# Kernel tuning notes

Hardware: AMD Instinct MI355X
Metric: run time of the kernel (lower is better)

Reference implementation:

```python
import jax, jax.numpy as jnp
import numpy as np

N = 100000
E = 1600000
H = 128
IN = 16
OUT = 16
L = 3
G = 256  # number of graphs
EPS = 1e-12


def setup_inputs() -> dict:
    key = jax.random.key(0)
    ks = jax.random.split(key, 24)
    s = 0.05
    inp = {
        "x": jax.random.normal(ks[0], (N, IN), jnp.float32),
        "pos": jax.random.normal(ks[1], (N, 3), jnp.float32),
        "edge_index": jax.random.randint(ks[2], (2, E), 0, N, jnp.int64),
        "batch": jnp.sort(jax.random.randint(ks[3], (N,), 0, G, jnp.int64)),
        # node_lin: Linear(IN,H), ReLU, Linear(H,H)
        "node_W1": jax.random.normal(ks[4], (IN, H), jnp.float32) * s,
        "node_b1": jnp.zeros((H,), jnp.float32),
        "node_W2": jax.random.normal(ks[5], (H, H), jnp.float32) * s,
        "node_b2": jnp.zeros((H,), jnp.float32),
        # per-layer local_nn: Linear(H+4,H), ReLU, Linear(H,H)  (stacked over L)
        "local_W1": jax.random.normal(ks[6], (L, H + 4, H), jnp.float32) * s,
        "local_b1": jnp.zeros((L, H), jnp.float32),
        "local_W2": jax.random.normal(ks[7], (L, H, H), jnp.float32) * s,
        "local_b2": jnp.zeros((L, H), jnp.float32),
        # per-layer global_nn: Linear(H,H), ReLU, Linear(H,H)
        "global_W1": jax.random.normal(ks[8], (L, H, H), jnp.float32) * s,
        "global_b1": jnp.zeros((L, H), jnp.float32),
        "global_W2": jax.random.normal(ks[9], (L, H, H), jnp.float32) * s,
        "global_b2": jnp.zeros((L, H), jnp.float32),
        # heads
        "lin1_W": jax.random.normal(ks[10], (H, H // 2), jnp.float32) * s,
        "lin1_b": jnp.zeros((H // 2,), jnp.float32),
        "lin2_W": jax.random.normal(ks[11], (H // 2, OUT), jnp.float32) * s,
        "lin2_b": jnp.zeros((OUT,), jnp.float32),
    }
    return inp


def _angle(v1, v2):
    c = jnp.cross(v1, v2, axis=1)
    return jnp.arctan2(jnp.linalg.norm(c, axis=1), jnp.sum(v1 * v2, axis=1))


def reference(x, pos, edge_index, batch,
              node_W1, node_b1, node_W2, node_b2,
              local_W1, local_b1, local_W2, local_b2,
              global_W1, global_b1, global_W2, global_b2,
              lin1_W, lin1_b, lin2_W, lin2_b):
    src = edge_index[0]  # j (source)
    dst = edge_index[1]  # i (target, aggregation index)

    normal = pos / (jnp.linalg.norm(pos, axis=-1, keepdims=True) + EPS)

    pos_i, pos_j = pos[dst], pos[src]
    n_i, n_j = normal[dst], normal[src]
    pseudo = pos_j - pos_i  # [E, 3]
    # point-pair features [E, 4] (constant across layers since pos is fixed)
    ppf = jnp.stack([
        jnp.linalg.norm(pseudo, axis=1),
        _angle(n_i, pseudo),
        _angle(n_j, pseudo),
        _angle(n_i, n_j),
    ], axis=1)

    # node_lin (x is 2D -> MLP path; embedding path unused)
    h = jax.nn.relu(x @ node_W1 + node_b1) @ node_W2 + node_b2  # [N, H]

    for l in range(L):
        msg = jnp.concatenate([h[src], ppf], axis=1)  # [E, H+4]
        msg = jax.nn.relu(msg @ local_W1[l] + local_b1[l]) @ local_W2[l] + local_b2[l]
        agg = jax.ops.segment_sum(msg, dst, num_segments=N)  # scatter-add to nodes
        h = jax.nn.relu(agg @ global_W1[l] + global_b1[l]) @ global_W2[l] + global_b2[l]
        h = jax.nn.relu(h)

    out = jax.nn.relu(h @ lin1_W + lin1_b) @ lin2_W + lin2_b  # [N, OUT]
    return jax.ops.segment_sum(out, batch, num_segments=G)  # [G, OUT]
```

## Files before the change

kernel.cpp:

```cpp
#include <hip/hip_runtime.h>

#define NN 100000
#define NE 1600000
#define HD 128
#define NL 3
#define NG 256
#define NB 196
#define BCAP 56

typedef __attribute__((ext_vector_type(8))) short short8;
typedef __attribute__((ext_vector_type(4))) float floatx4;
typedef __attribute__((ext_vector_type(2))) _Float16 half2v;

static __device__ __forceinline__ unsigned short f2bf(float f) {
    unsigned int u = __float_as_uint(f);
    u += 0x7fffu + ((u >> 16) & 1u);
    return (unsigned short)(u >> 16);
}
static __device__ __forceinline__ float bf2f(unsigned short h) {
    return __uint_as_float(((unsigned int)h) << 16);
}
static __device__ __forceinline__ float angle3(float ax, float ay, float az,
                                               float bx, float by, float bz) {
    float cx = ay*bz - az*by;
    float cy = az*bx - ax*bz;
    float cz = ax*by - ay*bx;
    float cn = sqrtf(cx*cx + cy*cy + cz*cz);
    float d  = ax*bx + ay*by + az*bz;
    return atan2f(cn, d);
}

union U32H2 { unsigned int u; half2v h; };
static __device__ __forceinline__ half2v u2h(unsigned int x) { U32H2 t; t.u = x; return t.h; }
static __device__ __forceinline__ unsigned int h2u(half2v x) { U32H2 t; t.h = x; return t.u; }


struct PrepSrcs { const float* p[14]; };

__global__ void k_prep(PrepSrcs s, unsigned short* __restrict__ dst) {
    int mat = blockIdx.y;
    int N = (mat == 13) ? 64 : 128;
    int e = blockIdx.x * 256 + threadIdx.x;
    if (e >= N * 128) return;
    int n = e >> 7, k = e & 127;
    dst[mat * 16384 + n * 128 + k] = f2bf(s.p[mat][k * N + n]);
}


__global__ void k_pn(const float* __restrict__ pos, float4* __restrict__ pn, int n) {
    int i = blockIdx.x * blockDim.x + threadIdx.x;
    if (i >= n) return;
    float x = pos[3*i], y = pos[3*i+1], z = pos[3*i+2];
    float inv = 1.0f / (sqrtf(x*x + y*y + z*z) + 1e-12f);
    pn[2*i]   = make_float4(x, y, z, 0.0f);
    pn[2*i+1] = make_float4(x*inv, y*inv, z*inv, 0.0f);
}


__global__ __launch_bounds__(256) void k_bcount(const int* __restrict__ ei,
                                                int* __restrict__ bcnt, int e) {
    __shared__ int cnt[NB];
    int tid = threadIdx.x;
    for (int i = tid; i < NB; i += 256) cnt[i] = 0;
    __syncthreads();
    int i0 = blockIdx.x * 4096 + tid * 16;
    if (i0 < e) {
#pragma unroll
        for (int q = 0; q < 4; q++) {
            int4 d4 = *(const int4*)(ei + NE + i0 + q * 4);
            atomicAdd(&cnt[d4.x >> 9], 1);
            atomicAdd(&cnt[d4.y >> 9], 1);
            atomicAdd(&cnt[d4.z >> 9], 1);
            atomicAdd(&cnt[d4.w >> 9], 1);
        }
    }
    __syncthreads();
    for (int i = tid; i < NB; i += 256)
        if (cnt[i]) atomicAdd(&bcnt[i], cnt[i]);
}

__global__ void k_bscan(const int* __restrict__ bcnt, int* __restrict__ bbase,
                        int* __restrict__ bcursor, int* __restrict__ starts) {
    if (threadIdx.x == 0 && blockIdx.x == 0) {
        int acc = 0;
        for (int b = 0; b < NB; b++) {
            bbase[b] = acc; bcursor[b] = acc;
            acc += bcnt[b];
        }
        bbase[NB] = acc;
        starts[NN] = NE;
    }
}

__global__ __launch_bounds__(256) void k_bscatter(const int* __restrict__ ei,
                                                  int* __restrict__ bcursor,
                                                  unsigned int* __restrict__ bids, int e) {
    __shared__ int lcnt[NB];
    __shared__ unsigned int lbuf[NB * BCAP];
    int tid = threadIdx.x;
    for (int i = tid; i < NB; i += 256) lcnt[i] = 0;
    __syncthreads();
    int i0 = blockIdx.x * 4096 + tid * 16;
    if (i0 < e) {
#pragma unroll
        for (int q = 0; q < 4; q++) {
            int4 s4 = *(const int4*)(ei + i0 + q * 4);
            int4 d4 = *(const int4*)(ei + NE + i0 + q * 4);
            int ds[4] = {d4.x, d4.y, d4.z, d4.w};
            int ss[4] = {s4.x, s4.y, s4.z, s4.w};
#pragma unroll
            for (int r = 0; r < 4; r++) {
                int d = ds[r];
                int b = d >> 9;
                unsigned int w = ((unsigned int)(d & 511) << 17) | (unsigned int)ss[r];
                int pos = atomicAdd(&lcnt[b], 1);
                if (pos < BCAP) lbuf[b * BCAP + pos] = w;
                else { int p = atomicAdd(&bcursor[b], 1); bids[p] = w; }
            }
        }
    }
    __syncthreads();
    if (tid < NB) {
        int c = lcnt[tid];
        if (c > BCAP) c = BCAP;
        if (c > 0) {
            int base = atomicAdd(&bcursor[tid], c);
            for (int k = 0; k < c; k++) bids[base + k] = lbuf[tid * BCAP + k];
        }
    }
}

__global__ __launch_bounds__(256) void k_bfinal(const unsigned int* __restrict__ bids,
                                                const int* __restrict__ bbase,
                                                int* __restrict__ ssrc,
                                                int* __restrict__ sdst,
                                                int* __restrict__ starts,
                                                int* __restrict__ deg) {
    __shared__ int s1[512];
    __shared__ int s2[256];
    int tid = threadIdx.x;
    int b = blockIdx.x;
    int node0 = b << 9;
    int base0 = bbase[b];
    int cnt = bbase[b + 1] - base0;
    s1[2 * tid] = 0; s1[2 * tid + 1] = 0;
    __syncthreads();
    for (int j = tid; j < cnt; j += 256)
        atomicAdd(&s1[bids[base0 + j] >> 17], 1);
    __syncthreads();
    int a0 = s1[2 * tid], a1 = s1[2 * tid + 1];
    s2[tid] = a0 + a1;
    __syncthreads();
    for (int off = 1; off < 256; off <<= 1) {
        int v = (tid >= off) ? s2[tid - off] : 0;
        __syncthreads();
        s2[tid] += v;
        __syncthreads();
    }
    int pairBase = (tid ? s2[tid - 1] : 0);
    int e0 = base0 + pairBase;
    int e1 = e0 + a0;
    int n0 = node0 + 2 * tid;
    if (n0 < NN)     { starts[n0] = e0;     deg[n0] = a0; }
    if (n0 + 1 < NN) { starts[n0 + 1] = e1; deg[n0 + 1] = a1; }
    s1[2 * tid] = e0; s1[2 * tid + 1] = e1;
    __syncthreads();
    for (int j = tid; j < cnt; j += 256) {
        unsigned int w = bids[base0 + j];
        int loc = w >> 17;
        int src = (int)(w & 0x1ffffu);
        int p = atomicAdd(&s1[loc], 1);
        ssrc[p] = src;
        sdst[p] = node0 + loc;
    }
}

__global__ void k_ppf_sorted(const int* __restrict__ ssrc, const int* __restrict__ sdst,
                             const float4* __restrict__ pn,
                             uint2* __restrict__ sppf, int e) {
    int j = blockIdx.x * blockDim.x + threadIdx.x;
    if (j >= e) return;
    int s = ssrc[j];
    int d = sdst[j];
    float4 ps_ = pn[2*s], ns_ = pn[2*s+1];
    float4 pd_ = pn[2*d], nd_ = pn[2*d+1];
    float px = ps_.x - pd_.x;
    float py = ps_.y - pd_.y;
    float pz = ps_.z - pd_.z;
    float f0 = sqrtf(px*px + py*py + pz*pz);
    float f1 = angle3(nd_.x, nd_.y, nd_.z, px, py, pz);
    float f2 = angle3(ns_.x, ns_.y, ns_.z, px, py, pz);
    float f3 = angle3(nd_.x, nd_.y, nd_.z, ns_.x, ns_.y, ns_.z);
    half2v h01 = { (_Float16)f0, (_Float16)f1 };
    half2v h23 = { (_Float16)f2, (_Float16)f3 };
    uint2 w;
    w.x = h2u(h01);
    w.y = h2u(h23);
    sppf[j] = w;
}


__global__ void k_node_lin1(const float* __restrict__ x, const float* __restrict__ W1,
                            const float* __restrict__ b1, unsigned short* __restrict__ u, int n) {
    __shared__ float sW[16 * HD];
    __shared__ float sb[HD];
    __shared__ float sx[16 * 16];
    int tid = threadIdx.x;
    for (int idx = tid; idx < 16 * HD; idx += 256) sW[idx] = W1[idx];
    if (tid < HD) sb[tid] = b1[tid];
    int r0 = blockIdx.x * 16;
    for (int idx = tid; idx < 16 * 16; idx += 256) {
        int r = r0 + (idx >> 4);
        sx[idx] = (r < n) ? x[r * 16 + (idx & 15)] : 0.0f;
    }
    __syncthreads();
    int col = tid & 127;
    int rsub = tid >> 7;
    float wcol[16];
#pragma unroll
    for (int k = 0; k < 16; k++) wcol[k] = sW[k * HD + col];
    float bb = sb[col];
    for (int rr = rsub; rr < 16; rr += 2) {
        int r = r0 + rr;
        if (r >= n) break;
        float acc = bb;
#pragma unroll
        for (int k = 0; k < 16; k++) acc = fmaf(sx[rr * 16 + k], wcol[k], acc);
        u[r * HD + col] = f2bf(fmaxf(acc, 0.0f));
    }
}


template <int NC, int EPI>
__global__ __launch_bounds__(256, 2) void k_gemm128(
    const unsigned short* __restrict__ A, const unsigned short* __restrict__ Wt,
    const float* __restrict__ bias, const int* __restrict__ deg,
    const float* __restrict__ b2, unsigned short* __restrict__ out, int n) {
    constexpr int SK = 136;
    __shared__ unsigned short Bt[NC * SK];
    int tid = threadIdx.x;
    for (int idx = tid; idx < NC * 16; idx += 256) {
        int c = idx >> 4, k8 = idx & 15;
        *(short8*)&Bt[c * SK + k8 * 8] = ((const short8*)Wt)[idx];
    }
    __syncthreads();

    int wave = tid >> 6, lane = tid & 63;
    int quad = lane >> 4, m = lane & 15;
    int rowBase = blockIdx.x * 128 + wave * 32;

    short8 a[2][4];
#pragma unroll
    for (int rt = 0; rt < 2; rt++) {
        int r = rowBase + rt * 16 + m;
        int rc = (r < n) ? r : (n - 1);
        const unsigned short* ap = A + (size_t)rc * 128 + quad * 8;
#pragma unroll
        for (int s = 0; s < 4; s++) a[rt][s] = *(const short8*)(ap + s * 32);
    }

    constexpr int NT = NC / 16;
    floatx4 acc[2][NT];
    floatx4 z = {0.0f, 0.0f, 0.0f, 0.0f};
#pragma unroll
    for (int rt = 0; rt < 2; rt++)
#pragma unroll
        for (int ct = 0; ct < NT; ct++) acc[rt][ct] = z;

#pragma unroll
    for (int ct = 0; ct < NT; ct++) {
        const unsigned short* bp = &Bt[(ct * 16 + m) * SK + quad * 8];
#pragma unroll
        for (int s = 0; s < 4; s++) {
            short8 b = *(const short8*)(bp + s * 32);
            acc[0][ct] = __builtin_amdgcn_mfma_f32_16x16x32_bf16(a[0][s], b, acc[0][ct], 0, 0, 0);
            acc[1][ct] = __builtin_amdgcn_mfma_f32_16x16x32_bf16(a[1][s], b, acc[1][ct], 0, 0, 0);
        }
    }

    float dv[2][4];
    if (EPI == 2) {
#pragma unroll
        for (int rt = 0; rt < 2; rt++)
#pragma unroll
            for (int r = 0; r < 4; r++) {
                int orow = rowBase + rt * 16 + quad * 4 + r;
                dv[rt][r] = (orow < n) ? (float)deg[orow] : 0.0f;
            }
    }

#pragma unroll
    for (int ct = 0; ct < NT; ct++) {
        int col = ct * 16 + m;
        float bv = (EPI == 0) ? 0.0f : ((EPI == 2) ? b2[col] : bias[col]);
#pragma unroll
        for (int rt = 0; rt < 2; rt++) {
#pragma unroll
            for (int r = 0; r < 4; r++) {
                int orow = rowBase + rt * 16 + quad * 4 + r;
                if (orow < n) {
                    float v = acc[rt][ct][r];
                    if (EPI == 1 || EPI == 3) v += bv;
                    if (EPI == 2) v += dv[rt][r] * bv;
                    if (EPI == 3) v = fmaxf(v, 0.0f);
                    out[(size_t)orow * NC + col] = f2bf(v);
                }
            }
        }
    }
}


#define SKW 136
#define SKT 136

__global__ __launch_bounds__(256, 2) void k_gchain(
    const unsigned short* __restrict__ S, const unsigned short* __restrict__ W2t,
    const unsigned short* __restrict__ GW1t, const unsigned short* __restrict__ GW2t,
    const int* __restrict__ deg, const float* __restrict__ b2,
    const float* __restrict__ Gb1, const float* __restrict__ Gb2,
    unsigned short* __restrict__ out, int n) {
    __shared__ unsigned short LW[128 * SKW];
    __shared__ unsigned short LT[128 * SKT];
    __shared__ float sb2[128], sg1[128], sg2[128];
    int tid = threadIdx.x;
    if (tid < 128) { sb2[tid] = b2[tid]; sg1[tid] = Gb1[tid]; sg2[tid] = Gb2[tid]; }
    int wave = tid >> 6, lane = tid & 63, quad = lane >> 4, m = lane & 15;
    int rowBase = wave * 32;
    int gBase = blockIdx.x * 128;
    int rowC = rowBase + quad * 4;
    const unsigned short* Ws[3] = {W2t, GW1t, GW2t};
    floatx4 z = {0.0f, 0.0f, 0.0f, 0.0f};
    short8 a[2][4];
#pragma unroll
    for (int rt = 0; rt < 2; rt++) {
        int r = gBase + rowBase + rt * 16 + m;
        int rc = r < n ? r : n - 1;
        const unsigned short* ap = S + (size_t)rc * 128 + quad * 8;
#pragma unroll
        for (int s = 0; s < 4; s++) a[rt][s] = *(const short8*)(ap + s * 32);
    }
    float dvd[2][4];
#pragma unroll
    for (int rt = 0; rt < 2; rt++)
#pragma unroll
        for (int r = 0; r < 4; r++) {
            int gr = gBase + rowBase + rt * 16 + quad * 4 + r;
            dvd[rt][r] = (float)deg[gr < n ? gr : n - 1];
        }

#pragma unroll
    for (int st = 0; st < 3; st++) {
        for (int idx = tid; idx < 128 * 16; idx += 256) {
            int c = idx >> 4, k8 = idx & 15;
            *(short8*)&LW[c * SKW + k8 * 8] = ((const short8*)Ws[st])[idx];
        }
        if (st > 0) {
#pragma unroll
            for (int rt = 0; rt < 2; rt++) {
                const unsigned short* tp = &LT[(rowBase + rt * 16 + m) * SKT + quad * 8];
#pragma unroll
                for (int s = 0; s < 4; s++) a[rt][s] = *(const short8*)(tp + s * 32);
            }
        }
        __syncthreads();

        floatx4 acc[2][8];
#pragma unroll
        for (int rt = 0; rt < 2; rt++)
#pragma unroll
            for (int ct = 0; ct < 8; ct++) acc[rt][ct] = z;
#pragma unroll
        for (int ct = 0; ct < 8; ct++) {
            const unsigned short* bp = &LW[(ct * 16 + m) * SKW + quad * 8];
#pragma unroll
            for (int s = 0; s < 4; s++) {
                short8 b = *(const short8*)(bp + s * 32);
                acc[0][ct] = __builtin_amdgcn_mfma_f32_16x16x32_bf16(a[0][s], b, acc[0][ct], 0, 0, 0);
                acc[1][ct] = __builtin_amdgcn_mfma_f32_16x16x32_bf16(a[1][s], b, acc[1][ct], 0, 0, 0);
            }
        }
#pragma unroll
        for (int ct = 0; ct < 8; ct++) {
            int col = ct * 16 + m;
            float bb = (st == 0) ? sb2[col] : (st == 1 ? sg1[col] : sg2[col]);
#pragma unroll
            for (int rt = 0; rt < 2; rt++) {
#pragma unroll
                for (int r = 0; r < 4; r++) {
                    float v = acc[rt][ct][r];
                    if (st == 0) v += dvd[rt][r] * bb;
                    else v = fmaxf(v + bb, 0.0f);
                    int row = rowBase + rt * 16 + quad * 4 + r;
                    if (st < 2) {
                        LT[row * SKT + col] = f2bf(v);
                    } else {
                        int gr = gBase + row;
                        if (gr < n) out[(size_t)gr * 128 + col] = f2bf(v);
                    }
                }
            }
        }
        __syncthreads();
    }
}


#if __has_builtin(__builtin_amdgcn_fdot2)
#define HAVE_FDOT2 1
#else
#define HAVE_FDOT2 0
#endif

static __device__ __forceinline__ void agg_edge(unsigned int u, uint2 q,
                                                half2v wA0, half2v wB0, half2v wA1, half2v wB1,
                                                float2 bb, float& a0, float& a1) {
    float tlo = __uint_as_float(u << 16);
    float thi = __uint_as_float(u & 0xffff0000u);
#if HAVE_FDOT2
    half2v p01 = u2h(q.x), p23 = u2h(q.y);
    float g0 = __builtin_amdgcn_fdot2(p01, wA0,
               __builtin_amdgcn_fdot2(p23, wB0, bb.x + tlo, false), false);
    float g1 = __builtin_amdgcn_fdot2(p01, wA1,
               __builtin_amdgcn_fdot2(p23, wB1, bb.y + thi, false), false);
#else
    half2v p01 = u2h(q.x), p23 = u2h(q.y);
    float px = (float)p01.x, py = (float)p01.y, pz = (float)p23.x, pw = (float)p23.y;
    float g0 = fmaf(px, (float)wA0.x, fmaf(py, (float)wA0.y,
               fmaf(pz, (float)wB0.x, fmaf(pw, (float)wB0.y, bb.x + tlo))));
    float g1 = fmaf(px, (float)wA1.x, fmaf(py, (float)wA1.y,
               fmaf(pz, (float)wB1.x, fmaf(pw, (float)wB1.y, bb.y + thi))));
#endif
    a0 += fmaxf(g0, 0.0f);
    a1 += fmaxf(g1, 0.0f);
}

__global__ __launch_bounds__(256, 8) void k_agg(
    const int* __restrict__ starts, const int* __restrict__ ssrc,
    const uint2* __restrict__ sppf, const unsigned int* __restrict__ t,
    const float* __restrict__ W1p, const float* __restrict__ b1,
    unsigned int* __restrict__ S, int n) {
    int node = (blockIdx.x * 256 + threadIdx.x) >> 6;
    if (node >= n) return;
    int lane = threadIdx.x & 63;
    int c2 = lane * 2;
    float2 w0 = *(const float2*)(W1p + c2);
    float2 w1 = *(const float2*)(W1p + 128 + c2);
    float2 w2 = *(const float2*)(W1p + 256 + c2);
    float2 w3 = *(const float2*)(W1p + 384 + c2);
    float2 bb = *(const float2*)(b1 + c2);
    half2v wA0 = { (_Float16)w0.x, (_Float16)w1.x };
    half2v wB0 = { (_Float16)w2.x, (_Float16)w3.x };
    half2v wA1 = { (_Float16)w0.y, (_Float16)w1.y };
    half2v wB1 = { (_Float16)w2.y, (_Float16)w3.y };
    int e0 = __builtin_amdgcn_readfirstlane(starts[node]);
    int e1 = __builtin_amdgcn_readfirstlane(starts[node + 1]);
    float a0 = 0.0f, a1 = 0.0f;
    int e = e0;
    for (; e + 8 <= e1; e += 8) {
        int s0 = ssrc[e],     s1 = ssrc[e + 1], s2 = ssrc[e + 2], s3 = ssrc[e + 3];
        int s4 = ssrc[e + 4], s5 = ssrc[e + 5], s6 = ssrc[e + 6], s7 = ssrc[e + 7];
        uint2 q0 = sppf[e],     q1 = sppf[e + 1], q2 = sppf[e + 2], q3 = sppf[e + 3];
        uint2 q4 = sppf[e + 4], q5 = sppf[e + 5], q6 = sppf[e + 6], q7 = sppf[e + 7];
        unsigned int u0 = t[((unsigned)s0 << 6) | lane];
        unsigned int u1 = t[((unsigned)s1 << 6) | lane];
        unsigned int u2 = t[((unsigned)s2 << 6) | lane];
        unsigned int u3 = t[((unsigned)s3 << 6) | lane];
        unsigned int u4 = t[((unsigned)s4 << 6) | lane];
        unsigned int u5 = t[((unsigned)s5 << 6) | lane];
        unsigned int u6 = t[((unsigned)s6 << 6) | lane];
        unsigned int u7 = t[((unsigned)s7 << 6) | lane];
        agg_edge(u0, q0, wA0, wB0, wA1, wB1, bb, a0, a1);
        agg_edge(u1, q1, wA0, wB0, wA1, wB1, bb, a0, a1);
        agg_edge(u2, q2, wA0, wB0, wA1, wB1, bb, a0, a1);
        agg_edge(u3, q3, wA0, wB0, wA1, wB1, bb, a0, a1);
        agg_edge(u4, q4, wA0, wB0, wA1, wB1, bb, a0, a1);
        agg_edge(u5, q5, wA0, wB0, wA1, wB1, bb, a0, a1);
        agg_edge(u6, q6, wA0, wB0, wA1, wB1, bb, a0, a1);
        agg_edge(u7, q7, wA0, wB0, wA1, wB1, bb, a0, a1);
    }
    for (; e + 4 <= e1; e += 4) {
        int s0 = ssrc[e], s1 = ssrc[e + 1], s2 = ssrc[e + 2], s3 = ssrc[e + 3];
        uint2 q0 = sppf[e], q1 = sppf[e + 1], q2 = sppf[e + 2], q3 = sppf[e + 3];
        unsigned int u0 = t[((unsigned)s0 << 6) | lane];
        unsigned int u1 = t[((unsigned)s1 << 6) | lane];
        unsigned int u2 = t[((unsigned)s2 << 6) | lane];
        unsigned int u3 = t[((unsigned)s3 << 6) | lane];
        agg_edge(u0, q0, wA0, wB0, wA1, wB1, bb, a0, a1);
        agg_edge(u1, q1, wA0, wB0, wA1, wB1, bb, a0, a1);
        agg_edge(u2, q2, wA0, wB0, wA1, wB1, bb, a0, a1);
        agg_edge(u3, q3, wA0, wB0, wA1, wB1, bb, a0, a1);
    }
    for (; e < e1; e++) {
        int s0 = ssrc[e];
        uint2 q0 = sppf[e];
        unsigned int u0 = t[((unsigned)s0 << 6) | lane];
        agg_edge(u0, q0, wA0, wB0, wA1, wB1, bb, a0, a1);
    }
    unsigned int r = ((unsigned int)f2bf(a1) << 16) | f2bf(a0);
    S[(size_t)node * 64 + lane] = r;
}


__global__ void k_head2(const unsigned short* __restrict__ v, const float* __restrict__ W,
                        const float* __restrict__ b, const int* __restrict__ batch,
                        float* __restrict__ outg, int n) {
    __shared__ float sW[64 * 16];
    __shared__ float sb[16];
    __shared__ float sacc[64][17];
    __shared__ int sbid[64];
    int tid = threadIdx.x;
    for (int idx = tid; idx < 64 * 16; idx += 256) sW[idx] = W[idx];
    if (tid < 16) sb[tid] = b[tid];
    int r0 = blockIdx.x * 64;
    if (tid < 64) {
        int r = r0 + tid;
        sbid[tid] = (r < n) ? batch[r] : -1;
    }
    __syncthreads();
    int rl = tid >> 4, c = tid & 15;
#pragma unroll
    for (int i = 0; i < 4; i++) {
        int row = rl + i * 16;
        int r = r0 + row;
        float acc = 0.0f;
        if (r < n) {
            const unsigned int* vr = (const unsigned int*)(v + (size_t)r * 64);
            acc = sb[c];
#pragma unroll
            for (int k2 = 0; k2 < 32; k2++) {
                unsigned int u = vr[k2];
                acc = fmaf(__uint_as_float(u << 16), sW[(2 * k2) * 16 + c], acc);
                acc = fmaf(__uint_as_float(u & 0xffff0000u), sW[(2 * k2 + 1) * 16 + c], acc);
            }
        }
        sacc[row][c] = acc;
    }
    __syncthreads();
    if (tid < 16) {
        int cc = tid;
        float run = 0.0f;
        int cur = sbid[0];
        for (int row = 0; row < 64; row++) {
            int bid = sbid[row];
            if (bid != cur) {
                if (cur >= 0) atomicAdd(&outg[cur * 16 + cc], run);
                run = 0.0f;
                cur = bid;
            }
            run += sacc[row][cc];
        }
        if (cur >= 0) atomicAdd(&outg[cur * 16 + cc], run);
    }
}


extern "C" void kernel_launch(void* const* d_in, const int* in_sizes, int n_in,
                              void* d_out, int out_size, void* d_ws, size_t ws_size,
                              hipStream_t stream) {
    (void)in_sizes; (void)n_in; (void)out_size; (void)ws_size;
    const float* x    = (const float*)d_in[0];
    const float* pos  = (const float*)d_in[1];
    const int*   ei   = (const int*)d_in[2];
    const int*   batch= (const int*)d_in[3];
    const float* nW1  = (const float*)d_in[4];
    const float* nb1  = (const float*)d_in[5];
    const float* nW2  = (const float*)d_in[6];
    const float* nb2  = (const float*)d_in[7];
    const float* lW1  = (const float*)d_in[8];
    const float* lb1  = (const float*)d_in[9];
    const float* lW2  = (const float*)d_in[10];
    const float* lb2  = (const float*)d_in[11];
    const float* gW1  = (const float*)d_in[12];
    const float* gb1  = (const float*)d_in[13];
    const float* gW2  = (const float*)d_in[14];
    const float* gb2  = (const float*)d_in[15];
    const float* l1W  = (const float*)d_in[16];
    const float* l1b  = (const float*)d_in[17];
    const float* l2W  = (const float*)d_in[18];
    const float* l2b  = (const float*)d_in[19];
    float* outg = (float*)d_out;

    char* ws = (char*)d_ws;
    size_t off = 0;
    auto alloc = [&](size_t bytes) -> void* {
        void* p = ws + off;
        off = (off + bytes + 255) & ~(size_t)255;
        return p;
    };
    unsigned short* P0 = (unsigned short*)alloc((size_t)NN * HD * 2);
    unsigned short* P1 = (unsigned short*)alloc((size_t)NN * HD * 2);
    uint2* sppf  = (uint2*)alloc((size_t)NE * 8);
    int* ssrc    = (int*)alloc((size_t)NE * 4);
    int* sdst    = (int*)alloc((size_t)NE * 4);
    float4* pn   = (float4*)alloc((size_t)NN * 32);
    int* deg     = (int*)alloc((size_t)NN * 4);
    int* starts  = (int*)alloc((size_t)(NN + 2) * 4);
    int* bcnt    = (int*)alloc((size_t)(NB + 2) * 4);
    int* bbase   = (int*)alloc((size_t)(NB + 2) * 4);
    int* bcursor = (int*)alloc((size_t)(NB + 2) * 4);
    unsigned short* pw = (unsigned short*)alloc((size_t)14 * 16384 * 2);
    unsigned int* bids = (unsigned int*)P0;

    PrepSrcs ps;
    ps.p[0] = nW2;
    for (int l = 0; l < 3; l++) {
        ps.p[1 + l] = lW1 + (size_t)l * 132 * 128;
        ps.p[4 + l] = lW2 + (size_t)l * 16384;
        ps.p[7 + l] = gW1 + (size_t)l * 16384;
        ps.p[10 + l] = gW2 + (size_t)l * 16384;
    }
    ps.p[13] = l1W;

    hipMemsetAsync(bcnt, 0, (size_t)(NB + 2) * 4, stream);
    hipMemsetAsync(outg, 0, (size_t)NG * 16 * 4, stream);

    k_prep<<<dim3(64, 14), 256, 0, stream>>>(ps, pw);
    k_pn<<<(NN + 255) / 256, 256, 0, stream>>>(pos, pn, NN);
    const int NTILE = (NE + 4095) / 4096;
    k_bcount<<<NTILE, 256, 0, stream>>>(ei, bcnt, NE);
    k_bscan<<<1, 64, 0, stream>>>(bcnt, bbase, bcursor, starts);
    k_bscatter<<<NTILE, 256, 0, stream>>>(ei, bcursor, bids, NE);
    k_bfinal<<<NB, 256, 0, stream>>>(bids, bbase, ssrc, sdst, starts, deg);
    k_ppf_sorted<<<(NE + 255) / 256, 256, 0, stream>>>(ssrc, sdst, pn, sppf, NE);

    k_node_lin1<<<(NN + 15) / 16, 256, 0, stream>>>(x, nW1, nb1, P1, NN);
    const int GB = (NN + 127) / 128;
    k_gemm128<128, 1><<<GB, 256, 0, stream>>>(P1, pw, nb2, nullptr, nullptr, P0, NN);

    unsigned short* hbuf = P0;
    unsigned short* obuf = P1;
    const int AGB = (NN * 64 + 255) / 256;
    for (int l = 0; l < NL; l++) {
        const float* W1p = lW1 + (size_t)l * 132 * 128 + 128 * 128;
        const float* b1  = lb1 + l * 128;
        const float* b2  = lb2 + l * 128;
        const float* Gb1 = gb1 + l * 128;
        const float* Gb2 = gb2 + l * 128;
        const unsigned short* pwW1h = pw + (size_t)(1 + l) * 16384;
        const unsigned short* pwW2  = pw + (size_t)(4 + l) * 16384;
        const unsigned short* pwGW1 = pw + (size_t)(7 + l) * 16384;
        const unsigned short* pwGW2 = pw + (size_t)(10 + l) * 16384;
        k_gemm128<128, 0><<<GB, 256, 0, stream>>>(hbuf, pwW1h, nullptr, nullptr, nullptr, obuf, NN);
        k_agg<<<AGB, 256, 0, stream>>>(starts, ssrc, sppf, (const unsigned int*)obuf,
                                       W1p, b1, (unsigned int*)hbuf, NN);
        k_gchain<<<GB, 256, 0, stream>>>(hbuf, pwW2, pwGW1, pwGW2, deg, b2, Gb1, Gb2, obuf, NN);
        unsigned short* tmp = hbuf; hbuf = obuf; obuf = tmp;
    }
    k_gemm128<64, 3><<<GB, 256, 0, stream>>>(hbuf, pw + (size_t)13 * 16384, l1b,
                                             nullptr, nullptr, obuf, NN);
    k_head2<<<(NN + 63) / 64, 256, 0, stream>>>(obuf, l2W, l2b, batch, outg, NN);
}
```

Measured before the change: 551.2 us.

## Fuse next-layer W1 projection and head lin1 into generic chained GEMM kernel

Replaces the separate k_gemm128 launches with a templated k_chain kernel that runs a configurable sequence of 128-wide GEMM stages per row tile, keeping intermediates in shared memory. The next layer's W1 projection is folded into the end of the previous layer's global MLP chain, and the lin1 head is folded into the last layer's chain. The node_lin second linear is chained with layer 0's W1 projection. This removes several kernel launches and the global-memory round trips of intermediate activations, at the cost of more stages per block and biases now read from global memory inside the epilogue.

```diff
diff --git a/kernel.cpp b/kernel.cpp
--- a/kernel.cpp
+++ b/kernel.cpp
@@ -231,112 +231,32 @@
 }
 
 
-template <int NC, int EPI>
-__global__ __launch_bounds__(256, 2) void k_gemm128(
-    const unsigned short* __restrict__ A, const unsigned short* __restrict__ Wt,
-    const float* __restrict__ bias, const int* __restrict__ deg,
-    const float* __restrict__ b2, unsigned short* __restrict__ out, int n) {
-    constexpr int SK = 136;
-    __shared__ unsigned short Bt[NC * SK];
-    int tid = threadIdx.x;
-    for (int idx = tid; idx < NC * 16; idx += 256) {
-        int c = idx >> 4, k8 = idx & 15;
-        *(short8*)&Bt[c * SK + k8 * 8] = ((const short8*)Wt)[idx];
-    }
-    __syncthreads();
-
-    int wave = tid >> 6, lane = tid & 63;
-    int quad = lane >> 4, m = lane & 15;
-    int rowBase = blockIdx.x * 128 + wave * 32;
-
-    short8 a[2][4];
-#pragma unroll
-    for (int rt = 0; rt < 2; rt++) {
-        int r = rowBase + rt * 16 + m;
-        int rc = (r < n) ? r : (n - 1);
-        const unsigned short* ap = A + (size_t)rc * 128 + quad * 8;
-#pragma unroll
-        for (int s = 0; s < 4; s++) a[rt][s] = *(const short8*)(ap + s * 32);
-    }
-
-    constexpr int NT = NC / 16;
-    floatx4 acc[2][NT];
-    floatx4 z = {0.0f, 0.0f, 0.0f, 0.0f};
-#pragma unroll
-    for (int rt = 0; rt < 2; rt++)
-#pragma unroll
-        for (int ct = 0; ct < NT; ct++) acc[rt][ct] = z;
-
-#pragma unroll
-    for (int ct = 0; ct < NT; ct++) {
-        const unsigned short* bp = &Bt[(ct * 16 + m) * SK + quad * 8];
-#pragma unroll
-        for (int s = 0; s < 4; s++) {
-            short8 b = *(const short8*)(bp + s * 32);
-            acc[0][ct] = __builtin_amdgcn_mfma_f32_16x16x32_bf16(a[0][s], b, acc[0][ct], 0, 0, 0);
-            acc[1][ct] = __builtin_amdgcn_mfma_f32_16x16x32_bf16(a[1][s], b, acc[1][ct], 0, 0, 0);
-        }
-    }
-
-    float dv[2][4];
-    if (EPI == 2) {
-#pragma unroll
-        for (int rt = 0; rt < 2; rt++)
-#pragma unroll
-            for (int r = 0; r < 4; r++) {
-                int orow = rowBase + rt * 16 + quad * 4 + r;
-                dv[rt][r] = (orow < n) ? (float)deg[orow] : 0.0f;
-            }
-    }
-
-#pragma unroll
-    for (int ct = 0; ct < NT; ct++) {
-        int col = ct * 16 + m;
-        float bv = (EPI == 0) ? 0.0f : ((EPI == 2) ? b2[col] : bias[col]);
-#pragma unroll
-        for (int rt = 0; rt < 2; rt++) {
-#pragma unroll
-            for (int r = 0; r < 4; r++) {
-                int orow = rowBase + rt * 16 + quad * 4 + r;
-                if (orow < n) {
-                    float v = acc[rt][ct][r];
-                    if (EPI == 1 || EPI == 3) v += bv;
-                    if (EPI == 2) v += dv[rt][r] * bv;
-                    if (EPI == 3) v = fmaxf(v, 0.0f);
-                    out[(size_t)orow * NC + col] = f2bf(v);
-                }
-            }
-        }
-    }
-}
-
-
 #define SKW 136
 #define SKT 136
 
-__global__ __launch_bounds__(256, 2) void k_gchain(
-    const unsigned short* __restrict__ S, const unsigned short* __restrict__ W2t,
-    const unsigned short* __restrict__ GW1t, const unsigned short* __restrict__ GW2t,
-    const int* __restrict__ deg, const float* __restrict__ b2,
-    const float* __restrict__ Gb1, const float* __restrict__ Gb2,
-    unsigned short* __restrict__ out, int n) {
+struct ChainArgs {
+    const unsigned short* W[4];
+    const float* bias[4];
+    int epi[4];
+};
+
+template <int NS, int NCL>
+__global__ __launch_bounds__(256, 2) void k_chain(
+    const unsigned short* __restrict__ in, ChainArgs ca,
+    const int* __restrict__ deg, unsigned short* __restrict__ out, int n) {
     __shared__ unsigned short LW[128 * SKW];
     __shared__ unsigned short LT[128 * SKT];
-    __shared__ float sb2[128], sg1[128], sg2[128];
     int tid = threadIdx.x;
-    if (tid < 128) { sb2[tid] = b2[tid]; sg1[tid] = Gb1[tid]; sg2[tid] = Gb2[tid]; }
     int wave = tid >> 6, lane = tid & 63, quad = lane >> 4, m = lane & 15;
     int rowBase = wave * 32;
     int gBase = blockIdx.x * 128;
-    int rowC = rowBase + quad * 4;
-    const unsigned short* Ws[3] = {W2t, GW1t, GW2t};
     floatx4 z = {0.0f, 0.0f, 0.0f, 0.0f};
     short8 a[2][4];
 #pragma unroll
     for (int rt = 0; rt < 2; rt++) {
         int r = gBase + rowBase + rt * 16 + m;
         int rc = r < n ? r : n - 1;
-        const unsigned short* ap = S + (size_t)rc * 128 + quad * 8;
+        const unsigned short* ap = in + (size_t)rc * 128 + quad * 8;
 #pragma unroll
         for (int s = 0; s < 4; s++) a[rt][s] = *(const short8*)(ap + s * 32);
     }
@@ -350,10 +270,11 @@
         }
 
 #pragma unroll
-    for (int st = 0; st < 3; st++) {
-        for (int idx = tid; idx < 128 * 16; idx += 256) {
+    for (int st = 0; st < NS; st++) {
+        const int NC = (st == NS - 1) ? NCL : 128;
+        for (int idx = tid; idx < NC * 16; idx += 256) {
             int c = idx >> 4, k8 = idx & 15;
-            *(short8*)&LW[c * SKW + k8 * 8] = ((const short8*)Ws[st])[idx];
+            *(short8*)&LW[c * SKW + k8 * 8] = ((const short8*)ca.W[st])[idx];
         }
         if (st > 0) {
 #pragma unroll
@@ -371,7 +292,7 @@
 #pragma unroll
             for (int ct = 0; ct < 8; ct++) acc[rt][ct] = z;
 #pragma unroll
-        for (int ct = 0; ct < 8; ct++) {
+        for (int ct = 0; ct < NC / 16; ct++) {
             const unsigned short* bp = &LW[(ct * 16 + m) * SKW + quad * 8];
 #pragma unroll
             for (int s = 0; s < 4; s++) {
@@ -380,23 +301,27 @@
                 acc[1][ct] = __builtin_amdgcn_mfma_f32_16x16x32_bf16(a[1][s], b, acc[1][ct], 0, 0, 0);
             }
         }
-#pragma unroll
-        for (int ct = 0; ct < 8; ct++) {
+        int epi = ca.epi[st];
+        const float* bptr = ca.bias[st];
+#pragma unroll
+        for (int ct = 0; ct < NC / 16; ct++) {
             int col = ct * 16 + m;
-            float bb = (st == 0) ? sb2[col] : (st == 1 ? sg1[col] : sg2[col]);
+            float bv = epi ? bptr[col] : 0.0f;
 #pragma unroll
             for (int rt = 0; rt < 2; rt++) {
 #pragma unroll
                 for (int r = 0; r < 4; r++) {
                     float v = acc[rt][ct][r];
-                    if (st == 0) v += dvd[rt][r] * bb;
-                    else v = fmaxf(v + bb, 0.0f);
+                    if (epi == 1) v += bv;
+                    else if (epi == 2) v += dvd[rt][r] * bv;
+                    else if (epi == 3) v = fmaxf(v + bv, 0.0f);
+                    unsigned short bw = f2bf(v);
                     int row = rowBase + rt * 16 + quad * 4 + r;
-                    if (st < 2) {
-                        LT[row * SKT + col] = f2bf(v);
+                    if (st == NS - 1) {
+                        int gr = gBase + row;
+                        if (gr < n) out[(size_t)gr * NCL + col] = bw;
                     } else {
-                        int gr = gBase + row;
-                        if (gr < n) out[(size_t)gr * 128 + col] = f2bf(v);
+                        LT[row * SKT + col] = bw;
                     }
                 }
             }
@@ -625,29 +550,39 @@
     k_ppf_sorted<<<(NE + 255) / 256, 256, 0, stream>>>(ssrc, sdst, pn, sppf, NE);
 
     k_node_lin1<<<(NN + 15) / 16, 256, 0, stream>>>(x, nW1, nb1, P1, NN);
+
     const int GB = (NN + 127) / 128;
-    k_gemm128<128, 1><<<GB, 256, 0, stream>>>(P1, pw, nb2, nullptr, nullptr, P0, NN);
-
-    unsigned short* hbuf = P0;
-    unsigned short* obuf = P1;
     const int AGB = (NN * 64 + 255) / 256;
+
+    {
+        ChainArgs ca;
+        ca.W[0] = pw;                      ca.bias[0] = nb2;     ca.epi[0] = 1;
+        ca.W[1] = pw + (size_t)1 * 16384;  ca.bias[1] = nullptr; ca.epi[1] = 0;
+        ca.W[2] = nullptr; ca.bias[2] = nullptr; ca.epi[2] = 0;
+        ca.W[3] = nullptr; ca.bias[3] = nullptr; ca.epi[3] = 0;
+        k_chain<2, 128><<<GB, 256, 0, stream>>>(P1, ca, deg, P0, NN);
+    }
+
+    unsigned short* tbuf = P0;
+    unsigned short* sbuf = P1;
     for (int l = 0; l < NL; l++) {
         const float* W1p = lW1 + (size_t)l * 132 * 128 + 128 * 128;
         const float* b1  = lb1 + l * 128;
-        const float* b2  = lb2 + l * 128;
-        const float* Gb1 = gb1 + l * 128;
-        const float* Gb2 = gb2 + l * 128;
-        const unsigned short* pwW1h = pw + (size_t)(1 + l) * 16384;
-        const unsigned short* pwW2  = pw + (size_t)(4 + l) * 16384;
-        const unsigned short* pwGW1 = pw + (size_t)(7 + l) * 16384;
-        const unsigned short* pwGW2 = pw + (size_t)(10 + l) * 16384;
-        k_gemm128<128, 0><<<GB, 256, 0, stream>>>(hbuf, pwW1h, nullptr, nullptr, nullptr, obuf, NN);
-        k_agg<<<AGB, 256, 0, stream>>>(starts, ssrc, sppf, (const unsigned int*)obuf,
-                                       W1p, b1, (unsigned int*)hbuf, NN);
-        k_gchain<<<GB, 256, 0, stream>>>(hbuf, pwW2, pwGW1, pwGW2, deg, b2, Gb1, Gb2, obuf, NN);
-        unsigned short* tmp = hbuf; hbuf = obuf; obuf = tmp;
-    }
-    k_gemm128<64, 3><<<GB, 256, 0, stream>>>(hbuf, pw + (size_t)13 * 16384, l1b,
-                                             nullptr, nullptr, obuf, NN);
-    k_head2<<<(NN + 63) / 64, 256, 0, stream>>>(obuf, l2W, l2b, batch, outg, NN);
-}
+        k_agg<<<AGB, 256, 0, stream>>>(starts, ssrc, sppf, (const unsigned int*)tbuf,
+                                       W1p, b1, (unsigned int*)sbuf, NN);
+        ChainArgs ca;
+        ca.W[0] = pw + (size_t)(4 + l) * 16384;  ca.bias[0] = lb2 + l * 128; ca.epi[0] = 2;
+        ca.W[1] = pw + (size_t)(7 + l) * 16384;  ca.bias[1] = gb1 + l * 128; ca.epi[1] = 3;
+        ca.W[2] = pw + (size_t)(10 + l) * 16384; ca.bias[2] = gb2 + l * 128; ca.epi[2] = 3;
+        if (l < NL - 1) {
+            ca.W[3] = pw + (size_t)(2 + l) * 16384;
+            ca.bias[3] = nullptr; ca.epi[3] = 0;
+            k_chain<4, 128><<<GB, 256, 0, stream>>>(sbuf, ca, deg, tbuf, NN);
+        } else {
+            ca.W[3] = pw + (size_t)13 * 16384;
+            ca.bias[3] = l1b; ca.epi[3] = 3;
+            k_chain<4, 64><<<GB, 256, 0, stream>>>(sbuf, ca, deg, tbuf, NN);
+        }
+    }
+    k_head2<<<(NN + 63) / 64, 256, 0, stream>>>(tbuf, l2W, l2b, batch, outg, NN);
+}
```

Measured after the change: 597.6 us. 1.08x slower.
